# Performance work log

Hardware: AMD Instinct MI355X
Metric: run time of the kernel (lower is better)

The kernel has to match this reference:

```python
import jax, jax.numpy as jnp
import numpy as np

V, H, B, T, L, G = 32000, 256, 16, 128, 50, 8
BETA, GAMMA = 5.0, 2.0
ATOL = 1e-8  # torch.allclose(x, zeros) default atol (rtol term vanishes vs zero)


def setup_inputs() -> dict:
    key = jax.random.key(0)
    ks = jax.random.split(key, 17)
    u = 1.0 / np.sqrt(H)
    def U(k, shape):
        return jax.random.uniform(k, shape, jnp.float32, -u, u)
    return dict(
        recipe=jax.random.randint(ks[0], (B, T), 0, V),
        g=jax.random.randint(ks[1], (B, G), 0, V),
        ingr=jax.random.randint(ks[2], (B, L), 0, V),
        wv=jax.random.normal(ks[3], (V, H), jnp.float32) * 0.1,  # frozen word vectors
        w_ih=U(ks[4], (5 * H, H)),
        w_hh=U(ks[5], (5 * H, H)),
        b_ih=U(ks[6], (5 * H,)),
        b_hh=U(ks[7], (5 * H,)),
        Z=U(ks[8], (H, H)),
        Y=U(ks[9], (H, H)),
        U_g=U(ks[10], (H, H)),
        z_bias=U(ks[11], (H,)),
        y_bias=U(ks[12], (H,)),
        S=U(ks[13], (3, H)),
        P=U(ks[14], (H, H)),
        fcW=U(ks[15], (V, H)),
        fcb=U(ks[16], (V,)),
    )


def _cgru_forward(x, g_vec, E, w_ih, w_hh, b_ih, b_hh, Z, Y, U_g, z_bias, y_bias, S, P):
    # x: (B,T,H) batch_first; g_vec: (B,H); E: (B,L,H)
    ht0 = g_vec @ U_g.T                      # init_hidden
    a0 = jnp.zeros((x.shape[0], E.shape[1]), x.dtype)
    E0 = E                                   # (1-a)*E with a=0
    ot0 = jnp.zeros_like(x[:, 0])
    goal_term = g_vec @ Y.T + y_bias         # constant across steps

    def step(carry, x_t):
        ht, ot, a, E_new = carry
        is_zero = jnp.all(jnp.abs(x_t) <= ATOL)
        # --- cell ---
        gi = x_t @ w_ih.T + b_ih
        gh = ht @ w_hh.T + b_hh
        i_r, i_u, i_n, i_g, i_i = jnp.split(gi, 5, axis=1)
        h_r, h_u, h_n, h_g, h_i = jnp.split(gh, 5, axis=1)
        z_t = jax.nn.sigmoid(i_u + h_u)
        r_t = jax.nn.sigmoid(i_r + h_r)
        s_t = jax.nn.sigmoid(i_g + h_g)
        q_t = jax.nn.sigmoid(i_i + h_i)
        tmp = E_new.sum(axis=1)              # 'mlk -> mk'
        h_tilde = jnp.tanh(i_n + r_t * h_n + s_t * goal_term + q_t * (tmp @ Z.T + z_bias))
        ht2 = h_tilde + z_t * (ht - h_tilde)
        # --- attention read/write ---
        ref = jax.nn.softmax((BETA * ht2) @ S.T, axis=-1)   # (B,3)
        h_proj = ht2 @ P.T
        En = (1.0 - a)[:, :, None] * E
        alpha_n = jax.nn.softmax(GAMMA * jnp.einsum('mk,mlk->ml', h_proj, En), axis=-1)
        c_n = jnp.einsum('mlk,ml->mk', E, alpha_n)
        Eu = a[:, :, None] * E
        alpha_u = jax.nn.softmax(GAMMA * jnp.einsum('mk,mlk->ml', h_proj, Eu), axis=-1)
        c_u = jnp.einsum('mlk,ml->mk', E, alpha_u)
        out = ref[:, 0:1] * h_proj + ref[:, 1:2] * c_n + ref[:, 2:3] * c_u
        a2 = a + ref[:, 1:2] * alpha_n
        # skip update when input step is all-zero (faithful to torch.allclose guard)
        ht_o = jnp.where(is_zero, ht, ht2)
        ot_o = jnp.where(is_zero, ot, out)
        a_o = jnp.where(is_zero, a, a2)
        E_o = jnp.where(is_zero, E_new, En)
        return (ht_o, ot_o, a_o, E_o), ot_o

    (ht, ot, a, E_new), outs = jax.lax.scan(step, (ht0, ot0, a0, E0),
                                            jnp.transpose(x, (1, 0, 2)))
    output = jnp.transpose(outs, (1, 0, 2))  # back to batch_first (B,T,H)
    return output, ht, a, E_new


def reference(recipe, g, ingr, wv, w_ih, w_hh, b_ih, b_hh, Z, Y, U_g,
              z_bias, y_bias, S, P, fcW, fcb):
    recipe_embed = wv[recipe]           # (B,T,H)
    goal_embed = wv[g].sum(axis=1)      # (B,H)
    E = wv[ingr]                        # (B,L,H)
    output, ht, a, E_new = _cgru_forward(recipe_embed, goal_embed, E,
                                         w_ih, w_hh, b_ih, b_hh, Z, Y, U_g,
                                         z_bias, y_bias, S, P)
    logits = output @ fcW.T + fcb       # (B,T,V)
    return logits, ht, a, E_new
```

## Files before the change

kernel.cpp:

```cpp
#include <hip/hip_runtime.h>

#define Hd   256
#define Bd   16
#define Td   128
#define Ld   50
#define Vd   32000
#define G5H  1280

typedef __attribute__((ext_vector_type(8))) short short8v;
typedef __attribute__((ext_vector_type(4))) float f32x4;

__device__ __forceinline__ unsigned short f2bu(float f) {
  unsigned u = __float_as_uint(f);
  unsigned r = (u + 0x7fffu + ((u >> 16) & 1u)) >> 16;
  return (unsigned short)r;
}
__device__ __forceinline__ float bu2f(unsigned short b) {
  return __uint_as_float(((unsigned)b) << 16);
}
__device__ __forceinline__ float sigm(float x) { return 1.f / (1.f + __expf(-x)); }

__device__ __forceinline__ void st_devu(unsigned* p, unsigned v) {
  __hip_atomic_store(p, v, __ATOMIC_RELAXED, __HIP_MEMORY_SCOPE_AGENT);
}
__device__ __forceinline__ unsigned ld_devu(const unsigned* p) {
  return __hip_atomic_load((unsigned*)p, __ATOMIC_RELAXED, __HIP_MEMORY_SCOPE_AGENT);
}
__device__ __forceinline__ void st_devd(double* p, double v) {
  __hip_atomic_store(p, v, __ATOMIC_RELAXED, __HIP_MEMORY_SCOPE_AGENT);
}
__device__ __forceinline__ double ld_devd(const double* p) {
  return __hip_atomic_load((double*)p, __ATOMIC_RELAXED, __HIP_MEMORY_SCOPE_AGENT);
}
__device__ __forceinline__ double pk2(float a, float b) {
  union { double d; float2 f; } u; u.f = make_float2(a, b); return u.d;
}

__global__ __launch_bounds__(256) void conv_kernel(
    const float* __restrict__ wv, const float* __restrict__ w_ih,
    const float* __restrict__ fcW, const float* __restrict__ w_hh,
    const float* __restrict__ Zm, const float* __restrict__ Pm,
    unsigned short* __restrict__ wv_b, unsigned short* __restrict__ wih_b,
    unsigned short* __restrict__ fcw_b, unsigned short* __restrict__ whh_f,
    unsigned short* __restrict__ z_f, unsigned short* __restrict__ p_f)
{
  const long N0 = 2048000, N1 = N0 + 81920, N2 = N1 + 2048000;
  const long NW = 81920, NZ = 16384, NP = 16384;
  const long N5 = N2 + NW + NZ + NP;
  for (long idx = (long)blockIdx.x * blockDim.x + threadIdx.x; idx < N5;
       idx += (long)gridDim.x * blockDim.x) {
    if (idx < N2) {
      const float* src; unsigned short* dst; long off;
      if      (idx < N0) { src = wv;   dst = wv_b;  off = idx; }
      else if (idx < N1) { src = w_ih; dst = wih_b; off = idx - N0; }
      else               { src = fcW;  dst = fcw_b; off = idx - N1; }
      float4 v = *(const float4*)(src + off * 4);
      ushort4 o;
      o.x = f2bu(v.x); o.y = f2bu(v.y); o.z = f2bu(v.z); o.w = f2bu(v.w);
      *(ushort4*)(dst + off * 4) = o;
    } else {
      long u = idx - N2;
      const float* src; unsigned short* dst;
      if      (u < NW)      { src = w_hh; dst = whh_f; }
      else if (u < NW + NZ) { src = Zm;   dst = z_f;  u -= NW; }
      else                  { src = Pm;   dst = p_f;  u -= NW + NZ; }
      long frag = u >> 7;
      int g128 = (int)(u & 127);
      int lane = g128 >> 1, e0 = (g128 & 1) * 4;
      long T = frag >> 3; int ks = (int)(frag & 7);
      int lr = lane & 15, lg = lane >> 4;
      float4 v = *(const float4*)(src + (T * 16 + lr) * 256 + ks * 32 + lg * 8 + e0);
      ushort4 o;
      o.x = f2bu(v.x); o.y = f2bu(v.y); o.z = f2bu(v.z); o.w = f2bu(v.w);
      *(ushort4*)(dst + u * 4) = o;
    }
  }
}

__global__ __launch_bounds__(256) void prep_kernel(
    const int* __restrict__ g, const int* __restrict__ ingr,
// ... 65 lines not shown
  }
  const unsigned short* brow = Bmat + (size_t)(n0 + srow) * Hd;

  for (int k0 = 0; k0 < Hd; k0 += 64) {
#pragma unroll
    for (int c = 0; c < 4; ++c) {
      int k = shalf * 32 + c * 8;
      uint4 va = *(const uint4*)(arow + k0 + k);
      uint4 vb = *(const uint4*)(brow + k0 + k);
      int byo = (srow << 7) + ((k << 1) ^ ((srow & 7) << 4));
      *(uint4*)((char*)As + byo) = va;
      *(uint4*)((char*)Bs + byo) = vb;
    }
    __syncthreads();
#pragma unroll
    for (int kk = 0; kk < 2; ++kk) {
      short8v af[4], bfr[4];
      const int kb = kk * 32 + lg * 8;
#pragma unroll
      for (int i = 0; i < 4; ++i) {
        int ar = wm * 64 + i * 16 + lr;
        af[i] = *(const short8v*)((const char*)As + (ar << 7) + ((kb << 1) ^ ((ar & 7) << 4)));
        int br = wn * 64 + i * 16 + lr;
        bfr[i] = *(const short8v*)((const char*)Bs + (br << 7) + ((kb << 1) ^ ((br & 7) << 4)));
      }
#pragma unroll
      for (int i = 0; i < 4; ++i)
#pragma unroll
        for (int jj = 0; jj < 4; ++jj)
          acc[i][jj] = __builtin_amdgcn_mfma_f32_16x16x32_bf16(af[i], bfr[jj], acc[i][jj], 0, 0, 0);
    }
    __syncthreads();
  }
#pragma unroll
  for (int i = 0; i < 4; ++i)
#pragma unroll
    for (int jj = 0; jj < 4; ++jj) {
      int col = n0 + wn * 64 + jj * 16 + lr;
      float bv = bias[col];
#pragma unroll
      for (int r = 0; r < 4; ++r) {
        int row = m0 + wm * 64 + i * 16 + lg * 4 + r;
        float v = acc[i][jj][r] + bv;
        if (MODE == 0) {
          int tt = row >> 4, bb = row & 15;
          C[((size_t)(bb * Td + tt)) * G5H + col] = v;
        } else {
          C[(size_t)row * Vd + col] = v;
        }
      }
    }
}

#define RNN_SMEM 149440
__global__ __launch_bounds__(256, 1) void rnn_kernel(
    const unsigned short* __restrict__ whh_f, const unsigned short* __restrict__ z_f,
    const unsigned short* __restrict__ p_f, const float* __restrict__ b_hh,
    const float* __restrict__ Sm, const float* __restrict__ z_bias,
    const float* __restrict__ gi, const float* __restrict__ goal_ws,
    const float* __restrict__ E_ws, const float* __restrict__ sumE,
    const float* __restrict__ HT0,
    unsigned short* __restrict__ out_all, float* __restrict__ d_out,
    float* __restrict__ XBH, float* __restrict__ XBP, unsigned* __restrict__ FL)
{
  extern __shared__ char smem[];
  unsigned short* w_lds = (unsigned short*)(smem);
  unsigned short* z_lds = (unsigned short*)(smem + 81920);
  unsigned short* p_lds = (unsigned short*)(smem + 98304);
  unsigned short* E_lds = (unsigned short*)(smem + 114688);
  float* hrow  = (float*)(smem + 141088);
  float* hp    = (float*)(smem + 142112);
  float* gh    = (float*)(smem + 143136);
  float* zd    = (float*)(smem + 143776);
  float* se    = (float*)(smem + 143904);
  float* gl    = (float*)(smem + 144928);
  float* bh    = (float*)(smem + 145056);
  float* zb    = (float*)(smem + 145696);
  float* a_l   = (float*)(smem + 145824);
  float* d_l   = (float*)(smem + 146080);
  float* an_l  = (float*)(smem + 146336);
  float* au_l  = (float*)(smem + 146592);
  float* sd    = (float*)(smem + 146848);
  float* refl  = (float*)(smem + 146864);
  unsigned short* ht_hi = (unsigned short*)(smem + 146880);
  unsigned short* ht_lo = (unsigned short*)(smem + 147392);
  unsigned short* tp_hi = (unsigned short*)(smem + 147904);
  unsigned short* tp_lo = (unsigned short*)(smem + 148416);
  unsigned short* hs_hi = (unsigned short*)(smem + 148928);
  unsigned short* hs_lo = (unsigned short*)(smem + 148992);
  float* Sl    = (float*)(smem + 149056);

  const int b  = blockIdx.x >> 3;
  const int j  = blockIdx.x & 7;
  const int hc0 = j << 5;
  const int tid = threadIdx.x;
  const int lane = tid & 63, wid = tid >> 6;
  const int lr = lane & 15, lg = lane >> 4;
  unsigned* FLb = FL + (b << 5);

  for (int idx = tid; idx < 5120; idx += 256) {
    int f = idx >> 6, e = idx & 63;
    int q = f >> 3, ks = f & 7;
    int T = (q >> 1) * 16 + 2 * j + (q & 1);
    *(uint4*)(w_lds + ((size_t)f << 9) + e * 8) =
        *(const uint4*)(whh_f + (((size_t)T * 8 + ks) << 9) + e * 8);
  }
  for (int idx = tid; idx < 1024; idx += 256) {
    int f = idx >> 6, e = idx & 63;
    int q = f >> 3, ks = f & 7;
    int T = 2 * j + q;
    *(uint4*)(z_lds + ((size_t)f << 9) + e * 8) =
        *(const uint4*)(z_f + (((size_t)T * 8 + ks) << 9) + e * 8);
  }
  for (int idx = tid; idx < 1024; idx += 256) {
    int f = idx >> 6, e = idx & 63;
    *(uint4*)(p_lds + ((size_t)f << 9) + e * 8) =
        *(const uint4*)(p_f + (((size_t)f * 8 + j) << 9) + e * 8);
  }
  for (int idx = tid; idx < Ld * 256; idx += 256) {
    int l = idx >> 8, k = idx & 255;
    E_lds[l * 264 + k] = f2bu(E_ws[((size_t)(b * Ld + l) << 8) + k]);
  }
  if (tid < 160) bh[tid] = b_hh[((tid >> 5) << 8) + hc0 + (tid & 31)];
  if (tid < 96) Sl[tid] = Sm[((tid >> 5) << 8) + hc0 + (tid & 31)];
  if (tid < 32) {
    gl[tid] = goal_ws[(b << 8) + hc0 + tid];
    zb[tid] = z_bias[hc0 + tid];
  }
  if (tid < 256) {
    float s0 = sumE[(b << 8) + tid];
    se[tid] = s0;
    unsigned short hi = f2bu(s0);
    tp_hi[tid] = hi; tp_lo[tid] = f2bu(s0 - bu2f(hi));
    float h0 = HT0[(b << 8) + tid];
    hrow[tid] = h0;
    unsigned short hh = f2bu(h0);
    ht_hi[tid] = hh; ht_lo[tid] = f2bu(h0 - bu2f(hh));
  }
  if (tid < 64) a_l[tid] = 0.f;
  __syncthreads();

  for (int t = 0; t < Td; ++t) {
    const int par = t & 1;
    double* htpub = (double*)XBH + ((size_t)((par * 16 + b) * 8 + j)) * 16;
    const double* htr = (const double*)XBH + ((size_t)((par * 16 + b) * 8)) * 16;
    double* hppub = (double*)XBP + ((size_t)((par * 16 + b) * 8 + j)) * 132;
    const double* hpr = (const double*)XBP + ((size_t)((par * 16 + b) * 8)) * 132;
    float g_ir = 0.f, g_iu = 0.f, g_in = 0.f, g_ig = 0.f, g_ii = 0.f;
    if (tid < 32) {
      const float* gib = gi + ((size_t)(b * Td + t)) * G5H + hc0 + tid;
      g_ir = gib[0];    g_iu = gib[256];  g_in = gib[512];
      g_ig = gib[768];  g_ii = gib[1024];
    }
#pragma unroll
    for (int ti = 0; ti < 3; ++ti) {
      int q = wid * 3 + ti;
      const unsigned short* base = (q < 10) ? (w_lds + ((size_t)(q * 8) << 9))
                                            : (z_lds + ((size_t)((q - 10) * 8) << 9));
      const unsigned short* shi = (q < 10) ? ht_hi : tp_hi;
      const unsigned short* slo = (q < 10) ? ht_lo : tp_lo;
      f32x4 acc = (f32x4){0.f, 0.f, 0.f, 0.f};
#pragma unroll
      for (int ks = 0; ks < 8; ++ks) {
        short8v av = *(const short8v*)(base + ((size_t)ks << 9) + (lane << 3));
        short8v bv = (short8v){0, 0, 0, 0, 0, 0, 0, 0};
        if (lr < 2)
          bv = *(const short8v*)((lr == 0 ? shi : slo) + ks * 32 + (lg << 3));
        acc = __builtin_amdgcn_mfma_f32_16x16x32_bf16(av, bv, acc, 0, 0, 0);
      }
#pragma unroll
      for (int r = 0; r < 4; ++r) {
        float v = acc[r] + __shfl_xor(acc[r], 1);
        if (lr == 0) {
          int row = q * 16 + lg * 4 + r;
          if (q < 10) gh[row] = v; else zd[row - 160] = v;
        }
      }
    }
    __syncthreads();
    if (tid < 32) {
      int cl = tid;
      float hr = gh[cl]       + bh[cl];
      float hu = gh[32 + cl]  + bh[32 + cl];
      float hn = gh[64 + cl]  + bh[64 + cl];
      float hg = gh[96 + cl]  + bh[96 + cl];
      float hq = gh[128 + cl] + bh[128 + cl];
      float rt = sigm(g_ir + hr), zt = sigm(g_iu + hu);
      float st = sigm(g_ig + hg), qt = sigm(g_ii + hq);
      float htl = tanhf(g_in + rt * hn + st * gl[cl] + qt * (zd[cl] + zb[cl]));
      float prev = hrow[hc0 + cl];
      float h2 = htl + zt * (prev - htl);
      unsigned short hi = f2bu(h2);
      hs_hi[cl] = hi; hs_lo[cl] = f2bu(h2 - bu2f(hi));
      float p0 = Sl[cl] * h2, p1 = Sl[32 + cl] * h2, p2 = Sl[64 + cl] * h2;
      p0 += __shfl_xor(p0, 1);  p0 += __shfl_xor(p0, 2);  p0 += __shfl_xor(p0, 4);
      p0 += __shfl_xor(p0, 8);  p0 += __shfl_xor(p0, 16);
      p1 += __shfl_xor(p1, 1);  p1 += __shfl_xor(p1, 2);  p1 += __shfl_xor(p1, 4);
      p1 += __shfl_xor(p1, 8);  p1 += __shfl_xor(p1, 16);
      p2 += __shfl_xor(p2, 1);  p2 += __shfl_xor(p2, 2);  p2 += __shfl_xor(p2, 4);
      p2 += __shfl_xor(p2, 8);  p2 += __shfl_xor(p2, 16);
      float h2o = __shfl_xor(h2, 1);
      if (!(cl & 1)) st_devd(htpub + (cl >> 1), pk2(h2, h2o));
      if (cl == 0) {
        st_devd(hppub + 128, pk2(p0, p1));
        st_devd(hppub + 129, pk2(p2, 0.f));
      }
    }
    __syncthreads();
#pragma unroll
    for (int ti = 0; ti < 4; ++ti) {
      int q = wid * 4 + ti;
      short8v av = *(const short8v*)(p_lds + ((size_t)q << 9) + (lane << 3));
      short8v bv = (short8v){0, 0, 0, 0, 0, 0, 0, 0};
      if (lr < 2)
        bv = *(const short8v*)((lr == 0 ? hs_hi : hs_lo) + (lg << 3));
      f32x4 acc = (f32x4){0.f, 0.f, 0.f, 0.f};
      acc = __builtin_amdgcn_mfma_f32_16x16x32_bf16(av, bv, acc, 0, 0, 0);
      float vv[4];
#pragma unroll
      for (int r = 0; r < 4; ++r) vv[r] = acc[r] + __shfl_xor(acc[r], 1);
      if (lr == 0) {
        int row = q * 16 + lg * 4;
        st_devd(hppub + (row >> 1), pk2(vv[0], vv[1]));
        st_devd(hppub + (row >> 1) + 1, pk2(vv[2], vv[3]));
      }
    }
    asm volatile("s_waitcnt vmcnt(0)" ::: "memory");
    __syncthreads();
    if (tid == 0) st_devu(FLb + j, (unsigned)(t + 1));
    if (tid < 64) {
      unsigned tgt = (unsigned)(t + 1);
      int guard = 0;
      while (1) {
        unsigned v = (lane < 8) ? ld_devu(FLb + lane) : tgt;
        if (__all((int)(v >= tgt))) break;
        __builtin_amdgcn_s_sleep(1);
        if (++guard > (1 << 20)) break;
      }
    }
    __syncthreads();
    if (tid < 128) {
      union { double d; float2 f; } u0, u1, u2, u3, u4, u5, u6, u7;
      u0.d = ld_devd(hpr + 0 * 132 + tid);
      u1.d = ld_devd(hpr + 1 * 132 + tid);
      u2.d = ld_devd(hpr + 2 * 132 + tid);
      u3.d = ld_devd(hpr + 3 * 132 + tid);
      u4.d = ld_devd(hpr + 4 * 132 + tid);
      u5.d = ld_devd(hpr + 5 * 132 + tid);
      u6.d = ld_devd(hpr + 6 * 132 + tid);
      u7.d = ld_devd(hpr + 7 * 132 + tid);
      float slo = ((((((u0.f.x + u1.f.x) + u2.f.x) + u3.f.x) + u4.f.x) + u5.f.x)
                   + u6.f.x) + u7.f.x;
      float shi = ((((((u0.f.y + u1.f.y) + u2.f.y) + u3.f.y) + u4.f.y) + u5.f.y)
                   + u6.f.y) + u7.f.y;
      hp[2 * tid] = slo;
      hp[2 * tid + 1] = shi;
    } else if (tid < 131) {
      int w = tid - 128;
      float s = 0.f;
#pragma unroll
      for (int js = 0; js < 8; ++js) {
        union { double d; float2 f; } u;
        u.d = ld_devd(hpr + js * 132 + 128 + (w >> 1));
        s += (w & 1) ? u.f.y : u.f.x;
      }
      sd[w] = s;
    }
    __syncthreads();
    if (tid < 200) {
      int l = tid >> 2, q = tid & 3;
      const unsigned short* er = E_lds + l * 264 + (q << 6);
      const float* hq = hp + (q << 6);
      float p = 0.f;
#pragma unroll 8
      for (int i = 0; i < 32; ++i) {
        unsigned uu = *(const unsigned*)(er + 2 * i);
        float e0 = __uint_as_float(uu << 16);
        float e1 = __uint_as_float(uu & 0xffff0000u);
        p = fmaf(e0, hq[2 * i], p);
        p = fmaf(e1, hq[2 * i + 1], p);
      }
      p += __shfl_xor(p, 1); p += __shfl_xor(p, 2);
      if (q == 0) d_l[l] = p;
    } else if (tid == 224) {
      float s0 = 5.0f * sd[0], s1 = 5.0f * sd[1], s2 = 5.0f * sd[2];
      float m = fmaxf(s0, fmaxf(s1, s2));
      float e0 = __expf(s0 - m), e1 = __expf(s1 - m), e2 = __expf(s2 - m);
      float inv = 1.f / (e0 + e1 + e2);
      refl[0] = e0 * inv; refl[1] = e1 * inv; refl[2] = e2 * inv;
    }
    __syncthreads();
    if (tid < 128) {
      int which = tid >> 6;
      int l = tid & 63;
      float dv;
      if (which == 0) dv = (l < Ld) ? 2.0f * (1.f - a_l[l]) * d_l[l] : -3.4e38f;
      else            dv = (l < Ld) ? 2.0f * a_l[l] * d_l[l]         : -3.4e38f;
      float m = dv;
      m = fmaxf(m, __shfl_xor(m, 1));  m = fmaxf(m, __shfl_xor(m, 2));
      m = fmaxf(m, __shfl_xor(m, 4));  m = fmaxf(m, __shfl_xor(m, 8));
      m = fmaxf(m, __shfl_xor(m, 16)); m = fmaxf(m, __shfl_xor(m, 32));
      float e = (l < Ld) ? __expf(dv - m) : 0.f;
      float ss = e;
      ss += __shfl_xor(ss, 1);  ss += __shfl_xor(ss, 2);  ss += __shfl_xor(ss, 4);
      ss += __shfl_xor(ss, 8);  ss += __shfl_xor(ss, 16); ss += __shfl_xor(ss, 32);
      float al = e / ss;
      if (which == 0) an_l[l] = al; else au_l[l] = al;
    }
    __syncthreads();
    {
      int k = tid;
      float accn = 0.f, accu = 0.f, acct = 0.f;
#pragma unroll 10
      for (int l = 0; l < Ld; ++l) {
        float e = bu2f(E_lds[l * 264 + k]);
        accn = fmaf(an_l[l], e, accn);
        accu = fmaf(au_l[l], e, accu);
        acct = fmaf(a_l[l], e, acct);
      }
      float outv = refl[0] * hp[k] + refl[1] * accn + refl[2] * accu;
      float tn = se[k] - acct;
      unsigned short th = f2bu(tn);
      tp_hi[k] = th; tp_lo[k] = f2bu(tn - bu2f(th));
      if (j == 0) {
        out_all[(((b << 7) + t) << 8) + k] = f2bu(outv);
        if (t == Td - 1) {
          for (int l = 0; l < Ld; ++l) {
            size_t o = ((size_t)(b * Ld + l) << 8) + k;
            d_out[(size_t)65540896 + o] = (1.f - a_l[l]) * E_ws[o];
          }
        }
      }
    }
    __syncthreads();
    if (tid < Ld) {
      float na = a_l[tid] + refl[1] * an_l[tid];
      a_l[tid] = na;
      if (t == Td - 1 && j == 0) d_out[(size_t)65540096 + b * Ld + tid] = na;
    }
    __syncthreads();
    if (tid < 128) {
      union { double d; float2 f; } u;
      u.d = ld_devd(htr + (tid >> 4) * 16 + (tid & 15));
      int c0 = 2 * tid;
      float a0 = u.f.x, a1 = u.f.y;
      hrow[c0] = a0; hrow[c0 + 1] = a1;
      unsigned short h0 = f2bu(a0), h1 = f2bu(a1);
      ht_hi[c0] = h0;     ht_lo[c0] = f2bu(a0 - bu2f(h0));
      ht_hi[c0 + 1] = h1; ht_lo[c0 + 1] = f2bu(a1 - bu2f(h1));
      if (t == Td - 1 && j == 0) {
        d_out[(size_t)65536000 + (b << 8) + c0] = a0;
        d_out[(size_t)65536000 + (b << 8) + c0 + 1] = a1;
      }
    }
    __syncthreads();
  }
}

extern "C" void kernel_launch(void* const* d_in, const int* in_sizes, int n_in,
                              void* d_out, int out_size, void* d_ws, size_t ws_size,
                              hipStream_t stream)
{
  const int*   recipe = (const int*)d_in[0];
  const int*   g      = (const int*)d_in[1];
  const int*   ingr   = (const int*)d_in[2];
  const float* wv     = (const float*)d_in[3];
  const float* w_ih   = (const float*)d_in[4];
  const float* w_hh   = (const float*)d_in[5];
  const float* b_ih   = (const float*)d_in[6];
  const float* b_hh   = (const float*)d_in[7];
  const float* Z      = (const float*)d_in[8];
  const float* Y      = (const float*)d_in[9];
  const float* Ug     = (const float*)d_in[10];
  const float* z_bias = (const float*)d_in[11];
  const float* y_bias = (const float*)d_in[12];
  const float* S      = (const float*)d_in[13];
  const float* P      = (const float*)d_in[14];
  const float* fcW    = (const float*)d_in[15];
  const float* fcb    = (const float*)d_in[16];
  float* out = (float*)d_out;
  char* ws = (char*)d_ws;

  size_t off = 0;
  unsigned* FL             = (unsigned*)(ws + off);        off += 2048;
  float* XBH               = (float*)(ws + off);           off += 32768;
  float* XBP               = (float*)(ws + off);           off += 270336;
  unsigned short* wv_b     = (unsigned short*)(ws + off);  off += 16384000;
  unsigned short* wih_b    = (unsigned short*)(ws + off);  off += 655360;
  unsigned short* fcw_b    = (unsigned short*)(ws + off);  off += 16384000;
  unsigned short* whh_f    = (unsigned short*)(ws + off);  off += 655360;
  unsigned short* z_f      = (unsigned short*)(ws + off);  off += 131072;
  unsigned short* p_f      = (unsigned short*)(ws + off);  off += 131072;
  float* gi_ws             = (float*)(ws + off);           off += 10485760;
  float* E_ws              = (float*)(ws + off);           off += 819200;
  float* sumE              = (float*)(ws + off);           off += 16384;
  float* goal_ws           = (float*)(ws + off);           off += 16384;
  float* HT0               = (float*)(ws + off);           off += 16384;
  unsigned short* out_all  = (unsigned short*)(ws + off);  off += 1048576;

  hipMemsetAsync(FL, 0, 2048, stream);
  conv_kernel<<<4096, 256, 0, stream>>>(wv, w_ih, fcW, w_hh, Z, P,
                                        wv_b, wih_b, fcw_b, whh_f, z_f, p_f);
  prep_kernel<<<16, 256, 0, stream>>>(g, ingr, wv, Ug, Y, y_bias,
                                      E_ws, sumE, goal_ws, HT0);
  gemm_bf16<0><<<dim3(16, 10), 256, 0, stream>>>(wv_b, wih_b, recipe, b_ih, gi_ws);
  hipFuncSetAttribute((const void*)rnn_kernel,
                      hipFuncAttributeMaxDynamicSharedMemorySize, RNN_SMEM);
  rnn_kernel<<<128, 256, RNN_SMEM, stream>>>(whh_f, z_f, p_f, b_hh, S, z_bias,
                                             gi_ws, goal_ws, E_ws, sumE, HT0,
                                             out_all, out, XBH, XBP, FL);
  gemm_bf16<1><<<dim3(16, 250), 256, 0, stream>>>(out_all, fcw_b, nullptr, fcb, out);
}
```

Before: 1.638 ms.

## Replace flag-based cross-block barrier with per-element tagged data exchange

```diff
diff --git a/kernel.cpp b/kernel.cpp
--- a/kernel.cpp
+++ b/kernel.cpp
@@ -20,12 +20,6 @@
 }
 __device__ __forceinline__ float sigm(float x) { return 1.f / (1.f + __expf(-x)); }
 
-__device__ __forceinline__ void st_devu(unsigned* p, unsigned v) {
-  __hip_atomic_store(p, v, __ATOMIC_RELAXED, __HIP_MEMORY_SCOPE_AGENT);
-}
-__device__ __forceinline__ unsigned ld_devu(const unsigned* p) {
-  return __hip_atomic_load((unsigned*)p, __ATOMIC_RELAXED, __HIP_MEMORY_SCOPE_AGENT);
-}
 __device__ __forceinline__ void st_devd(double* p, double v) {
   __hip_atomic_store(p, v, __ATOMIC_RELAXED, __HIP_MEMORY_SCOPE_AGENT);
 }
@@ -206,7 +200,7 @@
     const float* __restrict__ E_ws, const float* __restrict__ sumE,
     const float* __restrict__ HT0,
     unsigned short* __restrict__ out_all, float* __restrict__ d_out,
-    float* __restrict__ XBH, float* __restrict__ XBP, unsigned* __restrict__ FL)
+    double* __restrict__ XBH, double* __restrict__ XBP)
 {
   extern __shared__ char smem[];
   unsigned short* w_lds = (unsigned short*)(smem);
@@ -241,7 +235,6 @@
   const int tid = threadIdx.x;
   const int lane = tid & 63, wid = tid >> 6;
   const int lr = lane & 15, lg = lane >> 4;
-  unsigned* FLb = FL + (b << 5);
 
   for (int idx = tid; idx < 5120; idx += 256) {
     int f = idx >> 6, e = idx & 63;
@@ -264,7 +257,7 @@
   }
   for (int idx = tid; idx < Ld * 256; idx += 256) {
     int l = idx >> 8, k = idx & 255;
-    E_lds[l * 264 + k] = f2bu(E_ws[((size_t)(b * Ld + l) << 8) + k]);
+    E_lds[l * 264 + k + 2 * (k >> 6)] = f2bu(E_ws[((size_t)(b * Ld + l) << 8) + k]);
   }
   if (tid < 160) bh[tid] = b_hh[((tid >> 5) << 8) + hc0 + (tid & 31)];
   if (tid < 96) Sl[tid] = Sm[((tid >> 5) << 8) + hc0 + (tid & 31)];
@@ -287,10 +280,12 @@
 
   for (int t = 0; t < Td; ++t) {
     const int par = t & 1;
-    double* htpub = (double*)XBH + ((size_t)((par * 16 + b) * 8 + j)) * 16;
-    const double* htr = (const double*)XBH + ((size_t)((par * 16 + b) * 8)) * 16;
-    double* hppub = (double*)XBP + ((size_t)((par * 16 + b) * 8 + j)) * 132;
-    const double* hpr = (const double*)XBP + ((size_t)((par * 16 + b) * 8)) * 132;
+    double* htpub = XBH + ((size_t)((par * 16 + b) * 8 + j)) * 32;
+    const double* htr = XBH + ((size_t)((par * 16 + b) * 8)) * 32;
+    double* hppub = XBP + ((size_t)((par * 16 + b) * 8 + j)) * 260;
+    const double* hpr = XBP + ((size_t)((par * 16 + b) * 8)) * 260;
+    const unsigned tagu = (unsigned)(t + 1);
+    const float tagf = __uint_as_float(tagu);
     float g_ir = 0.f, g_iu = 0.f, g_in = 0.f, g_ig = 0.f, g_ii = 0.f;
     if (tid < 32) {
       const float* gib = gi + ((size_t)(b * Td + t)) * G5H + hc0 + tid;
@@ -337,6 +332,7 @@
       float h2 = htl + zt * (prev - htl);
       unsigned short hi = f2bu(h2);
       hs_hi[cl] = hi; hs_lo[cl] = f2bu(h2 - bu2f(hi));
+      st_devd(htpub + cl, pk2(h2, tagf));
       float p0 = Sl[cl] * h2, p1 = Sl[32 + cl] * h2, p2 = Sl[64 + cl] * h2;
       p0 += __shfl_xor(p0, 1);  p0 += __shfl_xor(p0, 2);  p0 += __shfl_xor(p0, 4);
       p0 += __shfl_xor(p0, 8);  p0 += __shfl_xor(p0, 16);
@@ -344,11 +340,10 @@
       p1 += __shfl_xor(p1, 8);  p1 += __shfl_xor(p1, 16);
       p2 += __shfl_xor(p2, 1);  p2 += __shfl_xor(p2, 2);  p2 += __shfl_xor(p2, 4);
       p2 += __shfl_xor(p2, 8);  p2 += __shfl_xor(p2, 16);
-      float h2o = __shfl_xor(h2, 1);
-      if (!(cl & 1)) st_devd(htpub + (cl >> 1), pk2(h2, h2o));
       if (cl == 0) {
-        st_devd(hppub + 128, pk2(p0, p1));
-        st_devd(hppub + 129, pk2(p2, 0.f));
+        st_devd(hppub + 256, pk2(p0, tagf));
+        st_devd(hppub + 257, pk2(p1, tagf));
+        st_devd(hppub + 258, pk2(p2, tagf));
       }
     }
     __syncthreads();
@@ -366,55 +361,64 @@
       for (int r = 0; r < 4; ++r) vv[r] = acc[r] + __shfl_xor(acc[r], 1);
       if (lr == 0) {
         int row = q * 16 + lg * 4;
-        st_devd(hppub + (row >> 1), pk2(vv[0], vv[1]));
-        st_devd(hppub + (row >> 1) + 1, pk2(vv[2], vv[3]));
-      }
-    }
-    asm volatile("s_waitcnt vmcnt(0)" ::: "memory");
-    __syncthreads();
-    if (tid == 0) st_devu(FLb + j, (unsigned)(t + 1));
-    if (tid < 64) {
-      unsigned tgt = (unsigned)(t + 1);
+        st_devd(hppub + row + 0, pk2(vv[0], tagf));
+        st_devd(hppub + row + 1, pk2(vv[1], tagf));
+        st_devd(hppub + row + 2, pk2(vv[2], tagf));
+        st_devd(hppub + row + 3, pk2(vv[3], tagf));
+      }
+    }
+    {
+      int e = tid;
+      float v[8];
+      bool got[8];
+#pragma unroll
+      for (int js = 0; js < 8; ++js) got[js] = false;
       int guard = 0;
       while (1) {
-        unsigned v = (lane < 8) ? ld_devu(FLb + lane) : tgt;
-        if (__all((int)(v >= tgt))) break;
+        bool ok = true;
+#pragma unroll
+        for (int js = 0; js < 8; ++js) {
+          if (!got[js]) {
+            union { double d; float2 f; } u;
+            u.d = ld_devd(hpr + (size_t)js * 260 + e);
+            if (__float_as_uint(u.f.y) == tagu) { v[js] = u.f.x; got[js] = true; }
+            else ok = false;
+          }
+        }
+        if (ok) break;
         __builtin_amdgcn_s_sleep(1);
         if (++guard > (1 << 20)) break;
       }
-    }
-    __syncthreads();
-    if (tid < 128) {
-      union { double d; float2 f; } u0, u1, u2, u3, u4, u5, u6, u7;
-      u0.d = ld_devd(hpr + 0 * 132 + tid);
-      u1.d = ld_devd(hpr + 1 * 132 + tid);
-      u2.d = ld_devd(hpr + 2 * 132 + tid);
-      u3.d = ld_devd(hpr + 3 * 132 + tid);
-      u4.d = ld_devd(hpr + 4 * 132 + tid);
-      u5.d = ld_devd(hpr + 5 * 132 + tid);
-      u6.d = ld_devd(hpr + 6 * 132 + tid);
-      u7.d = ld_devd(hpr + 7 * 132 + tid);
-      float slo = ((((((u0.f.x + u1.f.x) + u2.f.x) + u3.f.x) + u4.f.x) + u5.f.x)
-                   + u6.f.x) + u7.f.x;
-      float shi = ((((((u0.f.y + u1.f.y) + u2.f.y) + u3.f.y) + u4.f.y) + u5.f.y)
-                   + u6.f.y) + u7.f.y;
-      hp[2 * tid] = slo;
-      hp[2 * tid + 1] = shi;
-    } else if (tid < 131) {
-      int w = tid - 128;
-      float s = 0.f;
-#pragma unroll
-      for (int js = 0; js < 8; ++js) {
-        union { double d; float2 f; } u;
-        u.d = ld_devd(hpr + js * 132 + 128 + (w >> 1));
-        s += (w & 1) ? u.f.y : u.f.x;
-      }
-      sd[w] = s;
+      hp[e] = ((((((v[0] + v[1]) + v[2]) + v[3]) + v[4]) + v[5]) + v[6]) + v[7];
+      if (tid >= 253) {
+        int w = tid - 253;
+        float sv[8];
+        bool sgot[8];
+#pragma unroll
+        for (int js = 0; js < 8; ++js) sgot[js] = false;
+        int g2 = 0;
+        while (1) {
+          bool ok = true;
+#pragma unroll
+          for (int js = 0; js < 8; ++js) {
+            if (!sgot[js]) {
+              union { double d; float2 f; } u;
+              u.d = ld_devd(hpr + (size_t)js * 260 + 256 + w);
+              if (__float_as_uint(u.f.y) == tagu) { sv[js] = u.f.x; sgot[js] = true; }
+              else ok = false;
+            }
+          }
+          if (ok) break;
+          __builtin_amdgcn_s_sleep(1);
+          if (++g2 > (1 << 20)) break;
+        }
+        sd[w] = ((((((sv[0] + sv[1]) + sv[2]) + sv[3]) + sv[4]) + sv[5]) + sv[6]) + sv[7];
+      }
     }
     __syncthreads();
     if (tid < 200) {
       int l = tid >> 2, q = tid & 3;
-      const unsigned short* er = E_lds + l * 264 + (q << 6);
+      const unsigned short* er = E_lds + l * 264 + q * 66;
       const float* hq = hp + (q << 6);
       float p = 0.f;
 #pragma unroll 8
@@ -451,14 +455,37 @@
       ss += __shfl_xor(ss, 8);  ss += __shfl_xor(ss, 16); ss += __shfl_xor(ss, 32);
       float al = e / ss;
       if (which == 0) an_l[l] = al; else au_l[l] = al;
+    } else {
+      int idx = tid - 128;
+      int c0 = idx << 1;
+      float a0, a1;
+      int guard = 0;
+      while (1) {
+        union { double d; float2 f; } u0, u1;
+        u0.d = ld_devd(htr + c0);
+        u1.d = ld_devd(htr + c0 + 1);
+        a0 = u0.f.x; a1 = u1.f.x;
+        if (__float_as_uint(u0.f.y) == tagu && __float_as_uint(u1.f.y) == tagu) break;
+        __builtin_amdgcn_s_sleep(1);
+        if (++guard > (1 << 20)) break;
+      }
+      hrow[c0] = a0; hrow[c0 + 1] = a1;
+      unsigned short h0 = f2bu(a0), h1 = f2bu(a1);
+      ht_hi[c0] = h0;     ht_lo[c0] = f2bu(a0 - bu2f(h0));
+      ht_hi[c0 + 1] = h1; ht_lo[c0 + 1] = f2bu(a1 - bu2f(h1));
+      if (t == Td - 1 && j == 0) {
+        d_out[(size_t)65536000 + (b << 8) + c0] = a0;
+        d_out[(size_t)65536000 + (b << 8) + c0 + 1] = a1;
+      }
     }
     __syncthreads();
     {
       int k = tid;
+      int kp = k + 2 * (k >> 6);
       float accn = 0.f, accu = 0.f, acct = 0.f;
 #pragma unroll 10
       for (int l = 0; l < Ld; ++l) {
-        float e = bu2f(E_lds[l * 264 + k]);
+        float e = bu2f(E_lds[l * 264 + kp]);
         accn = fmaf(an_l[l], e, accn);
         accu = fmaf(au_l[l], e, accu);
         acct = fmaf(a_l[l], e, acct);
@@ -483,22 +510,6 @@
       a_l[tid] = na;
       if (t == Td - 1 && j == 0) d_out[(size_t)65540096 + b * Ld + tid] = na;
     }
-    __syncthreads();
-    if (tid < 128) {
-      union { double d; float2 f; } u;
-      u.d = ld_devd(htr + (tid >> 4) * 16 + (tid & 15));
-      int c0 = 2 * tid;
-      float a0 = u.f.x, a1 = u.f.y;
-      hrow[c0] = a0; hrow[c0 + 1] = a1;
-      unsigned short h0 = f2bu(a0), h1 = f2bu(a1);
-      ht_hi[c0] = h0;     ht_lo[c0] = f2bu(a0 - bu2f(h0));
-      ht_hi[c0 + 1] = h1; ht_lo[c0 + 1] = f2bu(a1 - bu2f(h1));
-      if (t == Td - 1 && j == 0) {
-        d_out[(size_t)65536000 + (b << 8) + c0] = a0;
-        d_out[(size_t)65536000 + (b << 8) + c0 + 1] = a1;
-      }
-    }
-    __syncthreads();
   }
 }
 
@@ -527,9 +538,8 @@
   char* ws = (char*)d_ws;
 
   size_t off = 0;
-  unsigned* FL             = (unsigned*)(ws + off);        off += 2048;
-  float* XBH               = (float*)(ws + off);           off += 32768;
-  float* XBP               = (float*)(ws + off);           off += 270336;
+  double* XBH              = (double*)(ws + off);          off += 65536;
+  double* XBP              = (double*)(ws + off);          off += 532480;
   unsigned short* wv_b     = (unsigned short*)(ws + off);  off += 16384000;
   unsigned short* wih_b    = (unsigned short*)(ws + off);  off += 655360;
   unsigned short* fcw_b    = (unsigned short*)(ws + off);  off += 16384000;
@@ -543,7 +553,7 @@
   float* HT0               = (float*)(ws + off);           off += 16384;
   unsigned short* out_all  = (unsigned short*)(ws + off);  off += 1048576;
 
-  hipMemsetAsync(FL, 0, 2048, stream);
+  hipMemsetAsync(XBH, 0, 65536 + 532480, stream);
   conv_kernel<<<4096, 256, 0, stream>>>(wv, w_ih, fcW, w_hh, Z, P,
                                         wv_b, wih_b, fcw_b, whh_f, z_f, p_f);
   prep_kernel<<<16, 256, 0, stream>>>(g, ingr, wv, Ug, Y, y_bias,
@@ -553,6 +563,6 @@
                       hipFuncAttributeMaxDynamicSharedMemorySize, RNN_SMEM);
   rnn_kernel<<<128, 256, RNN_SMEM, stream>>>(whh_f, z_f, p_f, b_hh, S, z_bias,
                                              gi_ws, goal_ws, E_ws, sumE, HT0,
-                                             out_all, out, XBH, XBP, FL);
+                                             out_all, out, XBH, XBP);
   gemm_bf16<1><<<dim3(16, 250), 256, 0, stream>>>(out_all, fcw_b, nullptr, fcb, out);
 }
```

Measured after the change: 1.799 ms. +9.8%, slower.

## Split W_hh matvec by input columns and publish partial gates across blocks

Applied to the files above, without the earlier changes.

```diff
diff --git a/kernel.cpp b/kernel.cpp
--- a/kernel.cpp
+++ b/kernel.cpp
@@ -197,8 +197,8 @@
     }
 }
 
-#define RNN_SMEM 149440
-__global__ __launch_bounds__(256, 1) void rnn_kernel(
+#define RNN_SMEM 147520
+__global__ __launch_bounds__(512, 1) void rnn_kernel(
     const unsigned short* __restrict__ whh_f, const unsigned short* __restrict__ z_f,
     const unsigned short* __restrict__ p_f, const float* __restrict__ b_hh,
     const float* __restrict__ Sm, const float* __restrict__ z_bias,
@@ -206,34 +206,33 @@
     const float* __restrict__ E_ws, const float* __restrict__ sumE,
     const float* __restrict__ HT0,
     unsigned short* __restrict__ out_all, float* __restrict__ d_out,
-    float* __restrict__ XBH, float* __restrict__ XBP, unsigned* __restrict__ FL)
+    double* __restrict__ XG, double* __restrict__ XP, double* __restrict__ XH,
+    unsigned* __restrict__ FL, unsigned* __restrict__ FLI)
 {
   extern __shared__ char smem[];
   unsigned short* w_lds = (unsigned short*)(smem);
   unsigned short* z_lds = (unsigned short*)(smem + 81920);
   unsigned short* p_lds = (unsigned short*)(smem + 98304);
   unsigned short* E_lds = (unsigned short*)(smem + 114688);
-  float* hrow  = (float*)(smem + 141088);
-  float* hp    = (float*)(smem + 142112);
-  float* gh    = (float*)(smem + 143136);
-  float* zd    = (float*)(smem + 143776);
-  float* se    = (float*)(smem + 143904);
-  float* gl    = (float*)(smem + 144928);
-  float* bh    = (float*)(smem + 145056);
-  float* zb    = (float*)(smem + 145696);
-  float* a_l   = (float*)(smem + 145824);
-  float* d_l   = (float*)(smem + 146080);
-  float* an_l  = (float*)(smem + 146336);
-  float* au_l  = (float*)(smem + 146592);
-  float* sd    = (float*)(smem + 146848);
-  float* refl  = (float*)(smem + 146864);
-  unsigned short* ht_hi = (unsigned short*)(smem + 146880);
-  unsigned short* ht_lo = (unsigned short*)(smem + 147392);
-  unsigned short* tp_hi = (unsigned short*)(smem + 147904);
-  unsigned short* tp_lo = (unsigned short*)(smem + 148416);
-  unsigned short* hs_hi = (unsigned short*)(smem + 148928);
-  unsigned short* hs_lo = (unsigned short*)(smem + 148992);
-  float* Sl    = (float*)(smem + 149056);
+  float* hp    = (float*)(smem + 141088);
+  float* gh_l  = (float*)(smem + 142112);
+  float* zd    = (float*)(smem + 142752);
+  float* se    = (float*)(smem + 142880);
+  float* gl    = (float*)(smem + 143904);
+  float* bh    = (float*)(smem + 144032);
+  float* zb    = (float*)(smem + 144672);
+  float* Sl    = (float*)(smem + 144800);
+  float* a_l   = (float*)(smem + 145184);
+  float* d_l   = (float*)(smem + 145440);
+  float* an_l  = (float*)(smem + 145696);
+  float* au_l  = (float*)(smem + 145952);
+  float* sd    = (float*)(smem + 146208);
+  float* refl  = (float*)(smem + 146224);
+  unsigned short* tp_hi = (unsigned short*)(smem + 146240);
+  unsigned short* tp_lo = (unsigned short*)(smem + 146752);
+  unsigned short* hs_hi = (unsigned short*)(smem + 147264);
+  unsigned short* hs_lo = (unsigned short*)(smem + 147328);
+  float* h_prev = (float*)(smem + 147392);
 
   const int b  = blockIdx.x >> 3;
   const int j  = blockIdx.x & 7;
@@ -241,100 +240,144 @@
   const int tid = threadIdx.x;
   const int lane = tid & 63, wid = tid >> 6;
   const int lr = lane & 15, lg = lane >> 4;
-  unsigned* FLb = FL + (b << 5);
-
-  for (int idx = tid; idx < 5120; idx += 256) {
+  unsigned* FLb  = FL + (b << 5);
+  unsigned* FLIb = FLI + (b << 5);
+
+  for (int idx = tid; idx < 5120; idx += 512) {
     int f = idx >> 6, e = idx & 63;
-    int q = f >> 3, ks = f & 7;
-    int T = (q >> 1) * 16 + 2 * j + (q & 1);
     *(uint4*)(w_lds + ((size_t)f << 9) + e * 8) =
-        *(const uint4*)(whh_f + (((size_t)T * 8 + ks) << 9) + e * 8);
-  }
-  for (int idx = tid; idx < 1024; idx += 256) {
+        *(const uint4*)(whh_f + (((size_t)f * 8 + j) << 9) + e * 8);
+  }
+  for (int idx = tid; idx < 1024; idx += 512) {
     int f = idx >> 6, e = idx & 63;
-    int q = f >> 3, ks = f & 7;
-    int T = 2 * j + q;
+    int T = 2 * j + (f >> 3), ks = f & 7;
     *(uint4*)(z_lds + ((size_t)f << 9) + e * 8) =
         *(const uint4*)(z_f + (((size_t)T * 8 + ks) << 9) + e * 8);
   }
-  for (int idx = tid; idx < 1024; idx += 256) {
+  for (int idx = tid; idx < 1024; idx += 512) {
     int f = idx >> 6, e = idx & 63;
     *(uint4*)(p_lds + ((size_t)f << 9) + e * 8) =
         *(const uint4*)(p_f + (((size_t)f * 8 + j) << 9) + e * 8);
   }
-  for (int idx = tid; idx < Ld * 256; idx += 256) {
+  for (int idx = tid; idx < Ld * 256; idx += 512) {
     int l = idx >> 8, k = idx & 255;
-    E_lds[l * 264 + k] = f2bu(E_ws[((size_t)(b * Ld + l) << 8) + k]);
+    E_lds[l * 264 + (k >> 5) * 33 + (k & 31)] =
+        f2bu(E_ws[((size_t)(b * Ld + l) << 8) + k]);
   }
   if (tid < 160) bh[tid] = b_hh[((tid >> 5) << 8) + hc0 + (tid & 31)];
   if (tid < 96) Sl[tid] = Sm[((tid >> 5) << 8) + hc0 + (tid & 31)];
   if (tid < 32) {
     gl[tid] = goal_ws[(b << 8) + hc0 + tid];
     zb[tid] = z_bias[hc0 + tid];
+    float h0 = HT0[(b << 8) + hc0 + tid];
+    h_prev[tid] = h0;
+    unsigned short hh = f2bu(h0);
+    hs_hi[tid] = hh; hs_lo[tid] = f2bu(h0 - bu2f(hh));
   }
   if (tid < 256) {
     float s0 = sumE[(b << 8) + tid];
     se[tid] = s0;
     unsigned short hi = f2bu(s0);
     tp_hi[tid] = hi; tp_lo[tid] = f2bu(s0 - bu2f(hi));
-    float h0 = HT0[(b << 8) + tid];
-    hrow[tid] = h0;
-    unsigned short hh = f2bu(h0);
-    ht_hi[tid] = hh; ht_lo[tid] = f2bu(h0 - bu2f(hh));
   }
   if (tid < 64) a_l[tid] = 0.f;
   __syncthreads();
 
+  {
+    double* XGp = XG + ((size_t)((0 * 16 + b) * 8 + j)) * 640;
+    short8v bv = (short8v){0,0,0,0,0,0,0,0};
+    if (lr < 2) bv = *(const short8v*)((lr == 0 ? hs_hi : hs_lo) + (lg << 3));
+#pragma unroll
+    for (int i = 0; i < 10; ++i) {
+      int T = wid * 10 + i;
+      short8v av = *(const short8v*)(w_lds + ((size_t)T << 9) + (lane << 3));
+      f32x4 acc = (f32x4){0.f, 0.f, 0.f, 0.f};
+      acc = __builtin_amdgcn_mfma_f32_16x16x32_bf16(av, bv, acc, 0, 0, 0);
+      float v0 = acc[0] + __shfl_xor(acc[0], 1);
+      float v1 = acc[1] + __shfl_xor(acc[1], 1);
+      float v2 = acc[2] + __shfl_xor(acc[2], 1);
+      float v3 = acc[3] + __shfl_xor(acc[3], 1);
+      if (lr == 0) {
+        st_devd(XGp + T * 8 + lg * 2, pk2(v0, v1));
+        st_devd(XGp + T * 8 + lg * 2 + 1, pk2(v2, v3));
+      }
+    }
+    asm volatile("s_waitcnt vmcnt(0)" ::: "memory");
+    __syncthreads();
+    if (tid == 0) st_devu(FLIb + j, 1u);
+  }
+
   for (int t = 0; t < Td; ++t) {
-    const int par = t & 1;
-    double* htpub = (double*)XBH + ((size_t)((par * 16 + b) * 8 + j)) * 16;
-    const double* htr = (const double*)XBH + ((size_t)((par * 16 + b) * 8)) * 16;
-    double* hppub = (double*)XBP + ((size_t)((par * 16 + b) * 8 + j)) * 132;
-    const double* hpr = (const double*)XBP + ((size_t)((par * 16 + b) * 8)) * 132;
+    const int par = t & 1, par1 = (t + 1) & 1;
+    const double* XGr = XG + ((size_t)((par * 16 + b) * 8)) * 640;
+    double* XGp = XG + ((size_t)((par1 * 16 + b) * 8 + j)) * 640;
+    double* XPp = XP + ((size_t)((par * 16 + b) * 8 + j)) * 132;
+    const double* XPr = XP + ((size_t)((par * 16 + b) * 8)) * 132;
+    if (t == 0) {
+      if (tid < 64) {
+        int guard = 0;
+        while (1) {
+          unsigned v = (lane < 8) ? ld_devu(FLIb + lane) : 1u;
+          if (__all((int)(v >= 1u))) break;
+          __builtin_amdgcn_s_sleep(1);
+          if (++guard > (1 << 20)) break;
+        }
+      }
+      __syncthreads();
+    }
     float g_ir = 0.f, g_iu = 0.f, g_in = 0.f, g_ig = 0.f, g_ii = 0.f;
     if (tid < 32) {
       const float* gib = gi + ((size_t)(b * Td + t)) * G5H + hc0 + tid;
       g_ir = gib[0];    g_iu = gib[256];  g_in = gib[512];
       g_ig = gib[768];  g_ii = gib[1024];
     }
-#pragma unroll
-    for (int ti = 0; ti < 3; ++ti) {
-      int q = wid * 3 + ti;
-      const unsigned short* base = (q < 10) ? (w_lds + ((size_t)(q * 8) << 9))
-                                            : (z_lds + ((size_t)((q - 10) * 8) << 9));
-      const unsigned short* shi = (q < 10) ? ht_hi : tp_hi;
-      const unsigned short* slo = (q < 10) ? ht_lo : tp_lo;
+    if (tid < 80) {
+      int g = tid >> 4, u = tid & 15;
+      int pr = g * 128 + (j << 4) + u;
+      float2 f0, f1, f2, f3, f4, f5, f6, f7;
+      { union { double d; float2 f; } u_;
+        u_.d = ld_devd(XGr + 0 * 640 + pr); f0 = u_.f;
+        u_.d = ld_devd(XGr + 1 * 640 + pr); f1 = u_.f;
+        u_.d = ld_devd(XGr + 2 * 640 + pr); f2 = u_.f;
+        u_.d = ld_devd(XGr + 3 * 640 + pr); f3 = u_.f;
+        u_.d = ld_devd(XGr + 4 * 640 + pr); f4 = u_.f;
+        u_.d = ld_devd(XGr + 5 * 640 + pr); f5 = u_.f;
+        u_.d = ld_devd(XGr + 6 * 640 + pr); f6 = u_.f;
+        u_.d = ld_devd(XGr + 7 * 640 + pr); f7 = u_.f; }
+      float sx = ((((((f0.x + f1.x) + f2.x) + f3.x) + f4.x) + f5.x) + f6.x) + f7.x;
+      float sy = ((((((f0.y + f1.y) + f2.y) + f3.y) + f4.y) + f5.y) + f6.y) + f7.y;
+      gh_l[g * 32 + 2 * u] = sx;
+      gh_l[g * 32 + 2 * u + 1] = sy;
+    } else if (wid == 4 || wid == 5) {
+      int tz = wid - 4;
       f32x4 acc = (f32x4){0.f, 0.f, 0.f, 0.f};
 #pragma unroll
       for (int ks = 0; ks < 8; ++ks) {
-        short8v av = *(const short8v*)(base + ((size_t)ks << 9) + (lane << 3));
-        short8v bv = (short8v){0, 0, 0, 0, 0, 0, 0, 0};
+        short8v av = *(const short8v*)(z_lds + ((size_t)(tz * 8 + ks) << 9) + (lane << 3));
+        short8v bv = (short8v){0,0,0,0,0,0,0,0};
         if (lr < 2)
-          bv = *(const short8v*)((lr == 0 ? shi : slo) + ks * 32 + (lg << 3));
+          bv = *(const short8v*)((lr == 0 ? tp_hi : tp_lo) + ks * 32 + (lg << 3));
         acc = __builtin_amdgcn_mfma_f32_16x16x32_bf16(av, bv, acc, 0, 0, 0);
       }
 #pragma unroll
       for (int r = 0; r < 4; ++r) {
         float v = acc[r] + __shfl_xor(acc[r], 1);
-        if (lr == 0) {
-          int row = q * 16 + lg * 4 + r;
-          if (q < 10) gh[row] = v; else zd[row - 160] = v;
-        }
+        if (lr == 0) zd[tz * 16 + lg * 4 + r] = v;
       }
     }
     __syncthreads();
     if (tid < 32) {
       int cl = tid;
-      float hr = gh[cl]       + bh[cl];
-      float hu = gh[32 + cl]  + bh[32 + cl];
-      float hn = gh[64 + cl]  + bh[64 + cl];
-      float hg = gh[96 + cl]  + bh[96 + cl];
-      float hq = gh[128 + cl] + bh[128 + cl];
+      float hr = gh_l[cl]       + bh[cl];
+      float hu = gh_l[32 + cl]  + bh[32 + cl];
+      float hn = gh_l[64 + cl]  + bh[64 + cl];
+      float hg = gh_l[96 + cl]  + bh[96 + cl];
+      float hq = gh_l[128 + cl] + bh[128 + cl];
       float rt = sigm(g_ir + hr), zt = sigm(g_iu + hu);
       float st = sigm(g_ig + hg), qt = sigm(g_ii + hq);
       float htl = tanhf(g_in + rt * hn + st * gl[cl] + qt * (zd[cl] + zb[cl]));
-      float prev = hrow[hc0 + cl];
-      float h2 = htl + zt * (prev - htl);
+      float h2 = htl + zt * (h_prev[cl] - htl);
+      h_prev[cl] = h2;
       unsigned short hi = f2bu(h2);
       hs_hi[cl] = hi; hs_lo[cl] = f2bu(h2 - bu2f(hi));
       float p0 = Sl[cl] * h2, p1 = Sl[32 + cl] * h2, p2 = Sl[64 + cl] * h2;
@@ -344,30 +387,51 @@
       p1 += __shfl_xor(p1, 8);  p1 += __shfl_xor(p1, 16);
       p2 += __shfl_xor(p2, 1);  p2 += __shfl_xor(p2, 2);  p2 += __shfl_xor(p2, 4);
       p2 += __shfl_xor(p2, 8);  p2 += __shfl_xor(p2, 16);
-      float h2o = __shfl_xor(h2, 1);
-      if (!(cl & 1)) st_devd(htpub + (cl >> 1), pk2(h2, h2o));
       if (cl == 0) {
-        st_devd(hppub + 128, pk2(p0, p1));
-        st_devd(hppub + 129, pk2(p2, 0.f));
-      }
-    }
-    __syncthreads();
-#pragma unroll
-    for (int ti = 0; ti < 4; ++ti) {
-      int q = wid * 4 + ti;
-      short8v av = *(const short8v*)(p_lds + ((size_t)q << 9) + (lane << 3));
-      short8v bv = (short8v){0, 0, 0, 0, 0, 0, 0, 0};
-      if (lr < 2)
-        bv = *(const short8v*)((lr == 0 ? hs_hi : hs_lo) + (lg << 3));
-      f32x4 acc = (f32x4){0.f, 0.f, 0.f, 0.f};
-      acc = __builtin_amdgcn_mfma_f32_16x16x32_bf16(av, bv, acc, 0, 0, 0);
-      float vv[4];
-#pragma unroll
-      for (int r = 0; r < 4; ++r) vv[r] = acc[r] + __shfl_xor(acc[r], 1);
-      if (lr == 0) {
-        int row = q * 16 + lg * 4;
-        st_devd(hppub + (row >> 1), pk2(vv[0], vv[1]));
-        st_devd(hppub + (row >> 1) + 1, pk2(vv[2], vv[3]));
+        st_devd(XPp + 128, pk2(p0, p1));
+        st_devd(XPp + 129, pk2(p2, 0.f));
+      }
+      if (t == Td - 1) {
+        float h2o = __shfl_xor(h2, 1);
+        if (!(cl & 1))
+          st_devd(XH + ((size_t)(b * 8 + j)) * 16 + (cl >> 1), pk2(h2, h2o));
+      }
+    }
+    __syncthreads();
+    {
+      short8v bv = (short8v){0,0,0,0,0,0,0,0};
+      if (lr < 2) bv = *(const short8v*)((lr == 0 ? hs_hi : hs_lo) + (lg << 3));
+      if (t < Td - 1) {
+#pragma unroll
+        for (int i = 0; i < 10; ++i) {
+          int T = wid * 10 + i;
+          short8v av = *(const short8v*)(w_lds + ((size_t)T << 9) + (lane << 3));
+          f32x4 acc = (f32x4){0.f, 0.f, 0.f, 0.f};
+          acc = __builtin_amdgcn_mfma_f32_16x16x32_bf16(av, bv, acc, 0, 0, 0);
+          float v0 = acc[0] + __shfl_xor(acc[0], 1);
+          float v1 = acc[1] + __shfl_xor(acc[1], 1);
+          float v2 = acc[2] + __shfl_xor(acc[2], 1);
+          float v3 = acc[3] + __shfl_xor(acc[3], 1);
+          if (lr == 0) {
+            st_devd(XGp + T * 8 + lg * 2, pk2(v0, v1));
+            st_devd(XGp + T * 8 + lg * 2 + 1, pk2(v2, v3));
+          }
+        }
+      }
+#pragma unroll
+      for (int qq = 0; qq < 2; ++qq) {
+        int q = wid * 2 + qq;
+        short8v av = *(const short8v*)(p_lds + ((size_t)q << 9) + (lane << 3));
+        f32x4 acc = (f32x4){0.f, 0.f, 0.f, 0.f};
+        acc = __builtin_amdgcn_mfma_f32_16x16x32_bf16(av, bv, acc, 0, 0, 0);
+        float v0 = acc[0] + __shfl_xor(acc[0], 1);
+        float v1 = acc[1] + __shfl_xor(acc[1], 1);
+        float v2 = acc[2] + __shfl_xor(acc[2], 1);
+        float v3 = acc[3] + __shfl_xor(acc[3], 1);
+        if (lr == 0) {
+          st_devd(XPp + q * 8 + lg * 2, pk2(v0, v1));
+          st_devd(XPp + q * 8 + lg * 2 + 1, pk2(v2, v3));
+        }
       }
     }
     asm volatile("s_waitcnt vmcnt(0)" ::: "memory");
@@ -385,49 +449,53 @@
     }
     __syncthreads();
     if (tid < 128) {
-      union { double d; float2 f; } u0, u1, u2, u3, u4, u5, u6, u7;
-      u0.d = ld_devd(hpr + 0 * 132 + tid);
-      u1.d = ld_devd(hpr + 1 * 132 + tid);
-      u2.d = ld_devd(hpr + 2 * 132 + tid);
-      u3.d = ld_devd(hpr + 3 * 132 + tid);
-      u4.d = ld_devd(hpr + 4 * 132 + tid);
-      u5.d = ld_devd(hpr + 5 * 132 + tid);
-      u6.d = ld_devd(hpr + 6 * 132 + tid);
-      u7.d = ld_devd(hpr + 7 * 132 + tid);
-      float slo = ((((((u0.f.x + u1.f.x) + u2.f.x) + u3.f.x) + u4.f.x) + u5.f.x)
-                   + u6.f.x) + u7.f.x;
-      float shi = ((((((u0.f.y + u1.f.y) + u2.f.y) + u3.f.y) + u4.f.y) + u5.f.y)
-                   + u6.f.y) + u7.f.y;
-      hp[2 * tid] = slo;
-      hp[2 * tid + 1] = shi;
-    } else if (tid < 131) {
+      float2 f0, f1, f2, f3, f4, f5, f6, f7;
+      { union { double d; float2 f; } u_;
+        u_.d = ld_devd(XPr + 0 * 132 + tid); f0 = u_.f;
+        u_.d = ld_devd(XPr + 1 * 132 + tid); f1 = u_.f;
+        u_.d = ld_devd(XPr + 2 * 132 + tid); f2 = u_.f;
+        u_.d = ld_devd(XPr + 3 * 132 + tid); f3 = u_.f;
+        u_.d = ld_devd(XPr + 4 * 132 + tid); f4 = u_.f;
+        u_.d = ld_devd(XPr + 5 * 132 + tid); f5 = u_.f;
+        u_.d = ld_devd(XPr + 6 * 132 + tid); f6 = u_.f;
+        u_.d = ld_devd(XPr + 7 * 132 + tid); f7 = u_.f; }
+      hp[2 * tid] =
+        ((((((f0.x + f1.x) + f2.x) + f3.x) + f4.x) + f5.x) + f6.x) + f7.x;
+      hp[2 * tid + 1] =
+        ((((((f0.y + f1.y) + f2.y) + f3.y) + f4.y) + f5.y) + f6.y) + f7.y;
+    } else if (tid == 128 || tid == 129) {
       int w = tid - 128;
-      float s = 0.f;
+      float2 f[8];
 #pragma unroll
       for (int js = 0; js < 8; ++js) {
-        union { double d; float2 f; } u;
-        u.d = ld_devd(hpr + js * 132 + 128 + (w >> 1));
-        s += (w & 1) ? u.f.y : u.f.x;
-      }
-      sd[w] = s;
-    }
-    __syncthreads();
-    if (tid < 200) {
-      int l = tid >> 2, q = tid & 3;
-      const unsigned short* er = E_lds + l * 264 + (q << 6);
-      const float* hq = hp + (q << 6);
+        union { double d; float2 f; } u_;
+        u_.d = ld_devd(XPr + js * 132 + 128 + w);
+        f[js] = u_.f;
+      }
+      float sx = ((((((f[0].x + f[1].x) + f[2].x) + f[3].x) + f[4].x) + f[5].x)
+                  + f[6].x) + f[7].x;
+      float sy = ((((((f[0].y + f[1].y) + f[2].y) + f[3].y) + f[4].y) + f[5].y)
+                  + f[6].y) + f[7].y;
+      if (w == 0) { sd[0] = sx; sd[1] = sy; }
+      else        { sd[2] = sx; }
+    }
+    __syncthreads();
+    if (tid < 400) {
+      int l = tid >> 3, sub = tid & 7;
+      const unsigned short* er = E_lds + l * 264 + sub * 33;
+      const float* hq = hp + (sub << 5);
       float p = 0.f;
 #pragma unroll 8
-      for (int i = 0; i < 32; ++i) {
+      for (int i = 0; i < 16; ++i) {
         unsigned uu = *(const unsigned*)(er + 2 * i);
         float e0 = __uint_as_float(uu << 16);
         float e1 = __uint_as_float(uu & 0xffff0000u);
         p = fmaf(e0, hq[2 * i], p);
         p = fmaf(e1, hq[2 * i + 1], p);
       }
-      p += __shfl_xor(p, 1); p += __shfl_xor(p, 2);
-      if (q == 0) d_l[l] = p;
-    } else if (tid == 224) {
+      p += __shfl_xor(p, 1); p += __shfl_xor(p, 2); p += __shfl_xor(p, 4);
+      if (sub == 0) d_l[l] = p;
+    } else if (tid == 448) {
       float s0 = 5.0f * sd[0], s1 = 5.0f * sd[1], s2 = 5.0f * sd[2];
       float m = fmaxf(s0, fmaxf(s1, s2));
       float e0 = __expf(s0 - m), e1 = __expf(s1 - m), e2 = __expf(s2 - m);
@@ -451,14 +519,22 @@
       ss += __shfl_xor(ss, 8);  ss += __shfl_xor(ss, 16); ss += __shfl_xor(ss, 32);
       float al = e / ss;
       if (which == 0) an_l[l] = al; else au_l[l] = al;
-    }
-    __syncthreads();
-    {
+    } else if (t == Td - 1 && j == 7 && tid >= 256 && tid < 384) {
+      int u = tid - 256;
+      int js = u >> 4, pi = u & 15;
+      union { double d; float2 f; } u_;
+      u_.d = ld_devd(XH + ((size_t)(b * 8 + js)) * 16 + pi);
+      d_out[(size_t)65536000 + (b << 8) + js * 32 + 2 * pi]     = u_.f.x;
+      d_out[(size_t)65536000 + (b << 8) + js * 32 + 2 * pi + 1] = u_.f.y;
+    }
+    __syncthreads();
+    if (tid < 256) {
       int k = tid;
+      int kp = (k >> 5) * 33 + (k & 31);
       float accn = 0.f, accu = 0.f, acct = 0.f;
 #pragma unroll 10
       for (int l = 0; l < Ld; ++l) {
-        float e = bu2f(E_lds[l * 264 + k]);
+        float e = bu2f(E_lds[l * 264 + kp]);
         accn = fmaf(an_l[l], e, accn);
         accu = fmaf(au_l[l], e, accu);
         acct = fmaf(a_l[l], e, acct);
@@ -467,7 +543,7 @@
       float tn = se[k] - acct;
       unsigned short th = f2bu(tn);
       tp_hi[k] = th; tp_lo[k] = f2bu(tn - bu2f(th));
-      if (j == 0) {
+      if ((t & 7) == j) {
         out_all[(((b << 7) + t) << 8) + k] = f2bu(outv);
         if (t == Td - 1) {
           for (int l = 0; l < Ld; ++l) {
@@ -481,22 +557,7 @@
     if (tid < Ld) {
       float na = a_l[tid] + refl[1] * an_l[tid];
       a_l[tid] = na;
-      if (t == Td - 1 && j == 0) d_out[(size_t)65540096 + b * Ld + tid] = na;
-    }
-    __syncthreads();
-    if (tid < 128) {
-      union { double d; float2 f; } u;
-      u.d = ld_devd(htr + (tid >> 4) * 16 + (tid & 15));
-      int c0 = 2 * tid;
-      float a0 = u.f.x, a1 = u.f.y;
-      hrow[c0] = a0; hrow[c0 + 1] = a1;
-      unsigned short h0 = f2bu(a0), h1 = f2bu(a1);
-      ht_hi[c0] = h0;     ht_lo[c0] = f2bu(a0 - bu2f(h0));
-      ht_hi[c0 + 1] = h1; ht_lo[c0 + 1] = f2bu(a1 - bu2f(h1));
-      if (t == Td - 1 && j == 0) {
-        d_out[(size_t)65536000 + (b << 8) + c0] = a0;
-        d_out[(size_t)65536000 + (b << 8) + c0 + 1] = a1;
-      }
+      if (t == Td - 1 && j == 7) d_out[(size_t)65540096 + b * Ld + tid] = na;
     }
     __syncthreads();
   }
@@ -528,8 +589,10 @@
 
   size_t off = 0;
   unsigned* FL             = (unsigned*)(ws + off);        off += 2048;
-  float* XBH               = (float*)(ws + off);           off += 32768;
-  float* XBP               = (float*)(ws + off);           off += 270336;
+  unsigned* FLI            = (unsigned*)(ws + off);        off += 2048;
+  double* XG               = (double*)(ws + off);          off += 1310720;
+  double* XP               = (double*)(ws + off);          off += 270336;
+  double* XH               = (double*)(ws + off);          off += 16384;
   unsigned short* wv_b     = (unsigned short*)(ws + off);  off += 16384000;
   unsigned short* wih_b    = (unsigned short*)(ws + off);  off += 655360;
   unsigned short* fcw_b    = (unsigned short*)(ws + off);  off += 16384000;
@@ -543,7 +606,7 @@
   float* HT0               = (float*)(ws + off);           off += 16384;
   unsigned short* out_all  = (unsigned short*)(ws + off);  off += 1048576;
 
-  hipMemsetAsync(FL, 0, 2048, stream);
+  hipMemsetAsync(FL, 0, 4096, stream);
   conv_kernel<<<4096, 256, 0, stream>>>(wv, w_ih, fcW, w_hh, Z, P,
                                         wv_b, wih_b, fcw_b, whh_f, z_f, p_f);
   prep_kernel<<<16, 256, 0, stream>>>(g, ingr, wv, Ug, Y, y_bias,
@@ -551,8 +614,8 @@
   gemm_bf16<0><<<dim3(16, 10), 256, 0, stream>>>(wv_b, wih_b, recipe, b_ih, gi_ws);
   hipFuncSetAttribute((const void*)rnn_kernel,
                       hipFuncAttributeMaxDynamicSharedMemorySize, RNN_SMEM);
-  rnn_kernel<<<128, 256, RNN_SMEM, stream>>>(whh_f, z_f, p_f, b_hh, S, z_bias,
+  rnn_kernel<<<128, 512, RNN_SMEM, stream>>>(whh_f, z_f, p_f, b_hh, S, z_bias,
                                              gi_ws, goal_ws, E_ws, sumE, HT0,
-                                             out_all, out, XBH, XBP, FL);
+                                             out_all, out, XG, XP, XH, FL, FLI);
   gemm_bf16<1><<<dim3(16, 250), 256, 0, stream>>>(out_all, fcw_b, nullptr, fcb, out);
 }
```

After: 1.827 ms. 1.12x slower.
